# Optimization experiments

Hardware: AMD Instinct MI355X
Metric: run time of the kernel (lower is better)

The kernel has to match this reference:

```python
import jax, jax.numpy as jnp
import numpy as np
from jax import lax


def loo_max(x):
    """Leave-one-out max over axis 1. x: (N, L, D) -> (N, L, D).
    Equivalent to torch's repeat + strip_main_diagonal + max(dim=2) without the
    (N, L, L, D) intermediate: for position i the LOO max is top1 unless i is
    the (unique chosen) argmax, in which case it is top2. With duplicates the
    second top-k value equals top1, so the result is still exact.
    """
    xt = jnp.swapaxes(x, 1, 2)                 # (N, D, L)
    top2, _ = lax.top_k(xt, 2)                 # (N, D, 2)
    amax = jnp.argmax(xt, axis=-1)             # (N, D)
    idx = jnp.arange(x.shape[1])[None, :, None]  # (1, L, 1)
    top1 = top2[..., 0][:, None, :]            # (N, 1, D)
    second = top2[..., 1][:, None, :]          # (N, 1, D)
    return jnp.where(idx == amax[:, None, :], second, top1)


def cross_max(y, from_length):
    """Plain max-pool over axis 1 of y, broadcast to (N, from_length, D)."""
    m = jnp.max(y, axis=1)                     # (N, D)
    return jnp.broadcast_to(m[:, None, :], (y.shape[0], from_length, y.shape[2]))


def setup_inputs() -> dict:
    key = jax.random.key(0)
    ks = jax.random.split(key, 6)
    N, L0, L1, D = 16, 2048, 1024, 128
    H = D + 2 * D  # in_dim + sum(in_dims) = 384
    scale = 1.0 / np.sqrt(H)
    return {
        "x0": jax.random.normal(ks[0], (N, L0, D), jnp.float32),
        "x1": jax.random.normal(ks[1], (N, L1, D), jnp.float32),
        "W0": jax.random.normal(ks[2], (D, H), jnp.float32) * scale,
        "b0": jax.random.normal(ks[3], (D,), jnp.float32) * scale,
        "W1": jax.random.normal(ks[4], (D, H), jnp.float32) * scale,
        "b1": jax.random.normal(ks[5], (D,), jnp.float32) * scale,
    }


def reference(x0, x1, W0, b0, W1, b1):
    L0, L1 = x0.shape[1], x1.shape[1]
    # group 0: [x0 | LOO-max(x0) | max(x1) broadcast] -> linear
    c0 = jnp.concatenate([x0, loo_max(x0), cross_max(x1, L0)], axis=-1)  # (N, L0, 384)
    y0 = jnp.einsum('nlh,oh->nlo', c0, W0) + b0                           # (N, L0, 128)
    # group 1: [x1 | max(x0) broadcast | LOO-max(x1)] -> linear
    c1 = jnp.concatenate([x1, cross_max(x0, L1), loo_max(x1)], axis=-1)  # (N, L1, 384)
    y1 = jnp.einsum('nlh,oh->nlo', c1, W1) + b1                           # (N, L1, 128)
    return (y0, y1)
```

## Files before the change

kernel.cpp:

```cpp
#include <hip/hip_runtime.h>
#include <hip/hip_bf16.h>

#define N_  16
#define L0_ 2048
#define L1_ 1024
#define D_  128
#define H_  384

#define PM1_0 0
#define PM2_0 65536
#define PAM_0 131072
#define PM1_1 196608
#define PM2_1 229376
#define PAM_1 262144
#define BASE_ 294912
#define WBF_  299008
#define HCNT_ 315392
#define HLIST_ 316160

typedef float  floatx4  __attribute__((ext_vector_type(4)));
typedef __bf16 bf16x8   __attribute__((ext_vector_type(8)));
typedef unsigned short ushortx8 __attribute__((ext_vector_type(8)));

__device__ __forceinline__ unsigned short f2bf(float f) {
  union { float f; unsigned int u; } v; v.f = f;
  unsigned int u = v.u;
  return (unsigned short)((u + 0x7fffu + ((u >> 16) & 1u)) >> 16);
}

__global__ __launch_bounds__(256) void stats_kernel(
    const float* __restrict__ x0, const float* __restrict__ x1,
    float* __restrict__ ws) {
  __shared__ float sm1[8][128], sm2[8][128];
  __shared__ int   sam[8][128];
  int bid = blockIdx.x, tid = threadIdx.x;
  const float* x; int n, chunk, L; float *pm1, *pm2; int* pam;
  if (bid < 512) {
    x = x0; n = bid >> 5; chunk = bid & 31; L = L0_;
    pm1 = ws + PM1_0; pm2 = ws + PM2_0; pam = (int*)ws + PAM_0;
  } else {
    int b = bid - 512;
    x = x1; n = b >> 4; chunk = b & 15; L = L1_;
    pm1 = ws + PM1_1; pm2 = ws + PM2_1; pam = (int*)ws + PAM_1;
  }
  int q = tid & 31, sub = tid >> 5;
  int lbase = chunk * 64 + sub * 8;
  const float* xp = x + (size_t)(n * L + lbase) * D_ + q * 4;

  float m1[4], m2[4]; int am[4];
#pragma unroll
  for (int j = 0; j < 4; j++) { m1[j] = -3.4e38f; m2[j] = -3.4e38f; am[j] = 0; }
#pragma unroll
  for (int r = 0; r < 8; r++) {
    float4 v = *(const float4*)(xp + (size_t)r * D_);
    float vv[4] = { v.x, v.y, v.z, v.w };
    int l = lbase + r;
#pragma unroll
    for (int j = 0; j < 4; j++) {
      if (vv[j] > m1[j]) { m2[j] = m1[j]; m1[j] = vv[j]; am[j] = l; }
      else if (vv[j] > m2[j]) m2[j] = vv[j];
    }
  }
#pragma unroll
  for (int j = 0; j < 4; j++) {
    int d = q * 4 + j;
    sm1[sub][d] = m1[j]; sm2[sub][d] = m2[j]; sam[sub][d] = am[j];
  }
  __syncthreads();
  if (tid < 128) {
    int d = tid;
    float M1 = sm1[0][d], M2 = sm2[0][d]; int AM = sam[0][d];
#pragma unroll
    for (int s = 1; s < 8; s++) {
      float c1 = sm1[s][d];
      if (c1 > M1) { M2 = fmaxf(M1, sm2[s][d]); M1 = c1; AM = sam[s][d]; }
      else M2 = fmaxf(M2, c1);
    }
    int idx = (chunk * N_ + n) * D_ + d;
    pm1[idx] = M1; pm2[idx] = M2; pam[idx] = AM;
  }
}

__global__ __launch_bounds__(256) void prep_kernel(
    const float* __restrict__ W0, const float* __restrict__ b0,
    const float* __restrict__ W1, const float* __restrict__ b1,
    float* __restrict__ ws) {
  __shared__ float t1a[128], t1b[128], sdl[128], bpart[128];
  __shared__ int   sam2[128], scnt[32];
  int bid = blockIdx.x, tid = threadIdx.x;
  int g = bid >> 4, n = bid & 15;
  const float* W = g ? W1 : W0;
  const float* bias = g ? b1 : b0;

  if (tid < 32) scnt[tid] = 0;

  if (tid < 128) {
    int d = tid;
    const float* pm1 = ws + PM1_0; const float* pm2 = ws + PM2_0;
    const int* pam = (int*)ws + PAM_0;
    float M1 = pm1[n * D_ + d], M2 = pm2[n * D_ + d]; int AM = pam[n * D_ + d];
    for (int c = 1; c < 32; c++) {
      int id2 = (c * N_ + n) * D_ + d;
      float c1 = pm1[id2];
      if (c1 > M1) { M2 = fmaxf(M1, pm2[id2]); M1 = c1; AM = pam[id2]; }
      else M2 = fmaxf(M2, c1);
    }
    t1a[d] = M1;
    if (g == 0) { sdl[d] = M2 - M1; sam2[d] = AM; }
  } else {
    int d = tid - 128;
    const float* pm1 = ws + PM1_1; const float* pm2 = ws + PM2_1;
    const int* pam = (int*)ws + PAM_1;
    float M1 = pm1[n * D_ + d], M2 = pm2[n * D_ + d]; int AM = pam[n * D_ + d];
    for (int c = 1; c < 16; c++) {
      int id2 = (c * N_ + n) * D_ + d;
      float c1 = pm1[id2];
      if (c1 > M1) { M2 = fmaxf(M1, pm2[id2]); M1 = c1; AM = pam[id2]; }
      else M2 = fmaxf(M2, c1);
    }
    t1b[d] = M1;
    if (g == 1) { sdl[d] = M2 - M1; sam2[d] = AM; }
  }
  __syncthreads();

  int o = tid & 127, half = tid >> 7;
  {
    const float* wr = W + (size_t)o * H_ + 128 + half * 128;
    const float* tv = half ? t1b : t1a;
    float bsum = 0.f;
#pragma unroll 4
    for (int d = 0; d < 128; d += 4) {
      float4 wv = *(const float4*)(wr + d);
      bsum += tv[d] * wv.x + tv[d + 1] * wv.y + tv[d + 2] * wv.z + tv[d + 3] * wv.w;
    }
    if (half) { bpart[o] = bsum; }
    __syncthreads();
    if (!half) ws[BASE_ + (g * N_ + n) * D_ + o] = bias[o] + bsum + bpart[o];
  }

  if (tid < 128) {
    int d = tid; int am = sam2[d]; float dl = sdl[d];
    int t = am >> 6;
    int slot = atomicAdd(&scnt[t], 1);
    int tile = (g == 0) ? (n * 32 + t) : (512 + n * 16 + t);
    int* hl = (int*)ws + HLIST_ + tile * 256;
    hl[slot * 2]     = (am & 63) | (d << 8);
    hl[slot * 2 + 1] = __float_as_int(dl);
  }
  __syncthreads();
  int tcount = g ? 16 : 32;
  if (tid < tcount) {
    int tile = (g == 0) ? (n * 32 + tid) : (512 + n * 16 + tid);
    ((int*)ws)[HCNT_ + tile] = scnt[tid];
  }

  if (n == 0) {
    unsigned short* wbf = (unsigned short*)(ws + WBF_) + g * 16384;
#pragma unroll
    for (int it = 0; it < 64; it++) {
      int f = tid + 256 * it;
      int oo = f >> 7, k = f & 127;
      wbf[f] = f2bf(W[(size_t)oo * H_ + k]);
    }
  }
}

__global__ __launch_bounds__(256) void gemm_kernel(
    const float* __restrict__ x0, const float* __restrict__ x1,
    const float* __restrict__ W0, const float* __restrict__ W1,
    float* __restrict__ out, const float* __restrict__ ws) {
  int bid = blockIdx.x, tid = threadIdx.x;
  int g, n, r0, L; const float *x, *W; float* y;
  if (bid < 512) { g = 0; n = bid >> 5; r0 = (bid & 31) << 6; L = L0_; x = x0; W = W0; y = out; }
  else { int b = bid - 512; g = 1; n = b >> 4; r0 = (b & 15) << 6; L = L1_; x = x1; W = W1;
         y = out + (size_t)N_ * L0_ * D_; }

  int w = tid >> 6, lane = tid & 63, lm = lane & 15, lq = lane >> 4;
  int rsub = (w & 1) << 5, cw = (w >> 1) << 6;

  int hc = ((const int*)ws)[HCNT_ + bid];
  const int* hl = (const int*)ws + HLIST_ + bid * 256;
  const float* bp = ws + BASE_ + (g * N_ + n) * D_;
  float bb[4];
#pragma unroll
  for (int j = 0; j < 4; j++) bb[j] = bp[cw + j * 16 + lm];

  const unsigned short* wbf = (const unsigned short*)(ws + WBF_) + g * 16384;
  const float* xb = x + (size_t)(n * L + r0 + rsub) * D_;

  floatx4 acc[2][4];
#pragma unroll
  for (int i = 0; i < 2; i++)
#pragma unroll
    for (int j = 0; j < 4; j++) acc[i][j] = (floatx4){0.f, 0.f, 0.f, 0.f};

#pragma unroll 1
  for (int kk = 0; kk < 4; kk++) {
    int ko = kk * 32 + lq * 8;
    bf16x8 af[2];
#pragma unroll
    for (int i = 0; i < 2; i++) {
      const float* p = xb + (size_t)(i * 16 + lm) * D_ + ko;
      float4 u = *(const float4*)p;
      float4 v = *(const float4*)(p + 4);
      ushortx8 t = { f2bf(u.x), f2bf(u.y), f2bf(u.z), f2bf(u.w),
                     f2bf(v.x), f2bf(v.y), f2bf(v.z), f2bf(v.w) };
      af[i] = __builtin_bit_cast(bf16x8, t);
    }
    bf16x8 bfr[4];
#pragma unroll
    for (int j = 0; j < 4; j++)
      bfr[j] = __builtin_bit_cast(bf16x8,
          *(const ushortx8*)&wbf[(cw + j * 16 + lm) * 128 + ko]);
#pragma unroll
    for (int i = 0; i < 2; i++)
#pragma unroll
      for (int j = 0; j < 4; j++)
        acc[i][j] = __builtin_amdgcn_mfma_f32_16x16x32_bf16(af[i], bfr[j], acc[i][j], 0, 0, 0);
  }

  int off = 128 + (g << 7);
  for (int k = 0; k < hc; k++) {
    int e = hl[2 * k]; float dl = __int_as_float(hl[2 * k + 1]);
    int row = e & 63, d = e >> 8;
    int rl = row - rsub;
    if (rl >= 0 && rl < 32 && ((rl >> 2) & 3) == lq) {
      int i = rl >> 4, rr = rl & 3;
#pragma unroll
      for (int j = 0; j < 4; j++)
        acc[i][j][rr] += dl * W[(size_t)(cw + j * 16 + lm) * H_ + off + d];
    }
  }

  float* yb = y + (size_t)(n * L + r0 + rsub) * D_;
#pragma unroll
  for (int i = 0; i < 2; i++)
#pragma unroll
    for (int j = 0; j < 4; j++)
#pragma unroll
      for (int r = 0; r < 4; r++)
        yb[(size_t)(i * 16 + lq * 4 + r) * D_ + cw + j * 16 + lm] = acc[i][j][r] + bb[j];
}

extern "C" void kernel_launch(void* const* d_in, const int* in_sizes, int n_in,
                              void* d_out, int out_size, void* d_ws, size_t ws_size,
                              hipStream_t stream) {
  const float* x0 = (const float*)d_in[0];
  const float* x1 = (const float*)d_in[1];
  const float* W0 = (const float*)d_in[2];
  const float* b0 = (const float*)d_in[3];
  const float* W1 = (const float*)d_in[4];
  const float* b1 = (const float*)d_in[5];
  float* out = (float*)d_out;
  float* ws  = (float*)d_ws;

  hipLaunchKernelGGL(stats_kernel, dim3(768), dim3(256), 0, stream, x0, x1, ws);
  hipLaunchKernelGGL(prep_kernel,  dim3(32),  dim3(256), 0, stream, W0, b0, W1, b1, ws);
  hipLaunchKernelGGL(gemm_kernel,  dim3(768), dim3(256), 0, stream,
                     x0, x1, W0, W1, out, ws);
}
```

Measured before the change: 136.2 us.

## Emit bf16 copy of x in stats pass and read it in GEMM

The stats kernel now converts each x row to bf16 and writes it to workspace while computing max statistics, so the GEMM reads half-width bf16 activations instead of re-reading fp32 and converting. The weight bf16 conversion moves from the tiny prep kernel into two extra blocks of the stats kernel, shortening the serial prep step. The GEMM k-loop is unrolled by two. This adds a bf16 write of x (half the fp32 size) in exchange for halving GEMM activation reads, so the net traffic gain depends on whether x reads were served from cache before.

```diff
diff --git a/kernel.cpp b/kernel.cpp
--- a/kernel.cpp
+++ b/kernel.cpp
@@ -17,10 +17,12 @@
 #define WBF_  299008
 #define HCNT_ 315392
 #define HLIST_ 316160
+#define XBF_  524288
 
 typedef float  floatx4  __attribute__((ext_vector_type(4)));
 typedef __bf16 bf16x8   __attribute__((ext_vector_type(8)));
 typedef unsigned short ushortx8 __attribute__((ext_vector_type(8)));
+typedef unsigned short ushortx4 __attribute__((ext_vector_type(4)));
 
 __device__ __forceinline__ unsigned short f2bf(float f) {
   union { float f; unsigned int u; } v; v.f = f;
@@ -30,22 +32,40 @@
 
 __global__ __launch_bounds__(256) void stats_kernel(
     const float* __restrict__ x0, const float* __restrict__ x1,
+    const float* __restrict__ W0, const float* __restrict__ W1,
     float* __restrict__ ws) {
   __shared__ float sm1[8][128], sm2[8][128];
   __shared__ int   sam[8][128];
   int bid = blockIdx.x, tid = threadIdx.x;
+
+  if (bid >= 768) {
+    int g = bid - 768;
+    const float* W = g ? W1 : W0;
+    unsigned short* wbf = (unsigned short*)(ws + WBF_) + g * 16384;
+#pragma unroll 4
+    for (int it = 0; it < 64; it++) {
+      int f = tid + 256 * it;
+      wbf[f] = f2bf(W[(size_t)(f >> 7) * H_ + (f & 127)]);
+    }
+    return;
+  }
+
   const float* x; int n, chunk, L; float *pm1, *pm2; int* pam;
+  unsigned short* xbf;
   if (bid < 512) {
     x = x0; n = bid >> 5; chunk = bid & 31; L = L0_;
     pm1 = ws + PM1_0; pm2 = ws + PM2_0; pam = (int*)ws + PAM_0;
+    xbf = (unsigned short*)(ws + XBF_);
   } else {
     int b = bid - 512;
     x = x1; n = b >> 4; chunk = b & 15; L = L1_;
     pm1 = ws + PM1_1; pm2 = ws + PM2_1; pam = (int*)ws + PAM_1;
+    xbf = (unsigned short*)(ws + XBF_) + (size_t)N_ * L0_ * D_;
   }
   int q = tid & 31, sub = tid >> 5;
   int lbase = chunk * 64 + sub * 8;
   const float* xp = x + (size_t)(n * L + lbase) * D_ + q * 4;
+  unsigned short* xbp = xbf + (size_t)(n * L + lbase) * D_ + q * 4;
 
   float m1[4], m2[4]; int am[4];
 #pragma unroll
@@ -54,6 +74,8 @@
   for (int r = 0; r < 8; r++) {
     float4 v = *(const float4*)(xp + (size_t)r * D_);
     float vv[4] = { v.x, v.y, v.z, v.w };
+    ushortx4 bv = { f2bf(v.x), f2bf(v.y), f2bf(v.z), f2bf(v.w) };
+    *(ushortx4*)(xbp + (size_t)r * D_) = bv;
     int l = lbase + r;
 #pragma unroll
     for (int j = 0; j < 4; j++) {
@@ -153,27 +175,21 @@
     int tile = (g == 0) ? (n * 32 + tid) : (512 + n * 16 + tid);
     ((int*)ws)[HCNT_ + tile] = scnt[tid];
   }
-
-  if (n == 0) {
-    unsigned short* wbf = (unsigned short*)(ws + WBF_) + g * 16384;
-#pragma unroll
-    for (int it = 0; it < 64; it++) {
-      int f = tid + 256 * it;
-      int oo = f >> 7, k = f & 127;
-      wbf[f] = f2bf(W[(size_t)oo * H_ + k]);
-    }
-  }
 }
 
 __global__ __launch_bounds__(256) void gemm_kernel(
-    const float* __restrict__ x0, const float* __restrict__ x1,
     const float* __restrict__ W0, const float* __restrict__ W1,
     float* __restrict__ out, const float* __restrict__ ws) {
   int bid = blockIdx.x, tid = threadIdx.x;
-  int g, n, r0, L; const float *x, *W; float* y;
-  if (bid < 512) { g = 0; n = bid >> 5; r0 = (bid & 31) << 6; L = L0_; x = x0; W = W0; y = out; }
-  else { int b = bid - 512; g = 1; n = b >> 4; r0 = (b & 15) << 6; L = L1_; x = x1; W = W1;
-         y = out + (size_t)N_ * L0_ * D_; }
+  int g, n, r0, L; const float* W; float* y; const unsigned short* xbf;
+  if (bid < 512) {
+    g = 0; n = bid >> 5; r0 = (bid & 31) << 6; L = L0_; W = W0; y = out;
+    xbf = (const unsigned short*)(ws + XBF_);
+  } else {
+    int b = bid - 512; g = 1; n = b >> 4; r0 = (b & 15) << 6; L = L1_; W = W1;
+    y = out + (size_t)N_ * L0_ * D_;
+    xbf = (const unsigned short*)(ws + XBF_) + (size_t)N_ * L0_ * D_;
+  }
 
   int w = tid >> 6, lane = tid & 63, lm = lane & 15, lq = lane >> 4;
   int rsub = (w & 1) << 5, cw = (w >> 1) << 6;
@@ -186,7 +202,7 @@
   for (int j = 0; j < 4; j++) bb[j] = bp[cw + j * 16 + lm];
 
   const unsigned short* wbf = (const unsigned short*)(ws + WBF_) + g * 16384;
-  const float* xb = x + (size_t)(n * L + r0 + rsub) * D_;
+  const unsigned short* xb = xbf + (size_t)(n * L + r0 + rsub) * D_;
 
   floatx4 acc[2][4];
 #pragma unroll
@@ -194,19 +210,14 @@
 #pragma unroll
     for (int j = 0; j < 4; j++) acc[i][j] = (floatx4){0.f, 0.f, 0.f, 0.f};
 
-#pragma unroll 1
+#pragma unroll 2
   for (int kk = 0; kk < 4; kk++) {
     int ko = kk * 32 + lq * 8;
     bf16x8 af[2];
 #pragma unroll
-    for (int i = 0; i < 2; i++) {
-      const float* p = xb + (size_t)(i * 16 + lm) * D_ + ko;
-      float4 u = *(const float4*)p;
-      float4 v = *(const float4*)(p + 4);
-      ushortx8 t = { f2bf(u.x), f2bf(u.y), f2bf(u.z), f2bf(u.w),
-                     f2bf(v.x), f2bf(v.y), f2bf(v.z), f2bf(v.w) };
-      af[i] = __builtin_bit_cast(bf16x8, t);
-    }
+    for (int i = 0; i < 2; i++)
+      af[i] = __builtin_bit_cast(bf16x8,
+          *(const ushortx8*)(xb + (size_t)(i * 16 + lm) * D_ + ko));
     bf16x8 bfr[4];
 #pragma unroll
     for (int j = 0; j < 4; j++)
@@ -254,8 +265,7 @@
   float* out = (float*)d_out;
   float* ws  = (float*)d_ws;
 
-  hipLaunchKernelGGL(stats_kernel, dim3(768), dim3(256), 0, stream, x0, x1, ws);
+  hipLaunchKernelGGL(stats_kernel, dim3(770), dim3(256), 0, stream, x0, x1, W0, W1, ws);
   hipLaunchKernelGGL(prep_kernel,  dim3(32),  dim3(256), 0, stream, W0, b0, W1, b1, ws);
-  hipLaunchKernelGGL(gemm_kernel,  dim3(768), dim3(256), 0, stream,
-                     x0, x1, W0, W1, out, ws);
-}
+  hipLaunchKernelGGL(gemm_kernel,  dim3(768), dim3(256), 0, stream, W0, W1, out, ws);
+}
```

Measured after the change: 140.4 us. 3.1% more time.
